# Performance work log

Measured on AMD Instinct MI355X. Metric: run time of the kernel, lower is better.

## Reference

```python
import jax, jax.numpy as jnp
import numpy as np
from jax import lax

EPS = 1e-5


def _bin_act(a):
    # sign binarization of activations (forward value only)
    return jnp.sign(a)


def _bin_weight(w):
    # XNOR-style: per-output-channel scaling alpha = mean(|w|), sign weights
    alpha = jnp.mean(jnp.abs(w), axis=(1, 2, 3), keepdims=True)  # [O,1,1,1]
    return jnp.sign(w) * alpha


def _binconv3x3(a, w, stride=1):
    ba = _bin_act(a)
    bw = _bin_weight(w)
    return lax.conv_general_dilated(
        ba, bw, window_strides=(stride, stride), padding=[(1, 1), (1, 1)],
        dimension_numbers=("NCHW", "OIHW", "NCHW"))


def _bn(x, gamma, beta, mean, var):
    # eval-mode BatchNorm2d with running stats; params shaped [1,C,1,1]
    inv = lax.rsqrt(var + EPS)
    return (x - mean) * inv * gamma + beta


def setup_inputs() -> dict:
    key = jax.random.key(0)
    ks = jax.random.split(key, 18)
    B, C, H, W = 32, 256, 56, 56
    p = lambda k, scale=1.0: jax.random.normal(k, (1, C, 1, 1), jnp.float32) * scale
    return {
        "x": jax.random.normal(ks[0], (B, C, H, W), jnp.float32),
        "sh11": p(ks[1], 0.01), "sh12": p(ks[2], 0.01),
        "w1": jax.random.normal(ks[3], (C, C, 3, 3), jnp.float32) * 0.05,
        "sc1": jax.random.uniform(ks[4], (1, C, 1, 1), jnp.float32) * 0.001,
        "g1": 1.0 + p(ks[5], 0.1), "b1": p(ks[6], 0.1),
        "m1": p(ks[7], 0.1), "v1": 0.5 + jax.random.uniform(ks[8], (1, C, 1, 1), jnp.float32),
        "sh21": p(ks[9], 0.01), "sh22": p(ks[10], 0.01),
        "w2": jax.random.normal(ks[11], (C, C, 3, 3), jnp.float32) * 0.05,
        "sc2": jax.random.uniform(ks[12], (1, C, 1, 1), jnp.float32) * 0.001,
        "g2": 1.0 + p(ks[13], 0.1), "b2": p(ks[14], 0.1),
        "m2": p(ks[15], 0.1), "v2": 0.5 + jax.random.uniform(ks[16], (1, C, 1, 1), jnp.float32),
    }


def reference(x, sh11, sh12, w1, sc1, g1, b1, m1, v1,
              sh21, sh22, w2, sc2, g2, b2, m2, v2):
    # --- sub-block 1 ---
    residual = x
    out1 = _binconv3x3(x + sh11, w1)
    out2 = _binconv3x3(x + sh12, w1)
    out = out1 + sc1 * out2
    out = _bn(out, g1, b1, m1, v1)
    out = out + residual
    out = jnp.clip(out, -1.0, 1.0)  # Hardtanh
    # --- sub-block 2 ---
    residual = out
    out1 = _binconv3x3(out + sh21, w2)
    out2 = _binconv3x3(out + sh22, w2)
    out = out1 + sc2 * out2
    out = _bn(out, g2, b2, m2, v2)
    out = out + residual
    out = jnp.clip(out, -1.0, 1.0)  # Hardtanh
    return out
```

## Files before the change

### kernel.cpp

```cpp
#include <hip/hip_runtime.h>
#include <cstdint>
#include <cstddef>

typedef int v4i __attribute__((ext_vector_type(4)));

#define HWSZ 3136
#define WID 56
#define CCH 256
#define BAT 32
#define NPIX (BAT*HWSZ)
#define KTOT 2304
#define PW 58
#define PIMG (PW*PW)
#define PSZ (BAT*PIMG*64)

static __device__ __forceinline__ uint16_t f2bf(float f) {
    uint32_t x = __float_as_uint(f);
    x += 0x7fffu + ((x >> 16) & 1u);
    return (uint16_t)(x >> 16);
}

static __device__ __forceinline__ void load_lds_16(const void* g, void* l) {
    __builtin_amdgcn_global_load_lds(
        (const __attribute__((address_space(1))) uint32_t*)g,
        (__attribute__((address_space(3))) uint32_t*)l, 16, 0, 0);
}

__global__ void pack_weights(const float* __restrict__ w,
                             const float* __restrict__ sc,
                             const float* __restrict__ g,
                             const float* __restrict__ bb,
                             const float* __restrict__ m,
                             const float* __restrict__ v,
                             int8_t* __restrict__ wpack,
                             float* __restrict__ params) {
    int o = blockIdx.x;
    int t = threadIdx.x;
    const float* wo = w + (size_t)o * KTOT;
    __shared__ float red[256];
    float s = 0.f;
    for (int i = t; i < KTOT; i += 256) {
        float val = wo[i];
        s += fabsf(val);
        int c = i / 9, tap = i - c * 9;
        int8_t sgn = (val > 0.f) ? 1 : ((val < 0.f) ? -1 : 0);
        wpack[(size_t)o * KTOT + tap * 256 + c] = sgn;
    }
    red[t] = s;
    __syncthreads();
    for (int off = 128; off > 0; off >>= 1) {
        if (t < off) red[t] += red[t + off];
        __syncthreads();
    }
    if (t == 0) {
        float alpha = red[0] / (float)KTOT;
        float inv = rsqrtf(v[o] + 1e-5f);
        float cs = alpha * inv * g[o];
        params[o]         = cs;
        params[256 + o]   = cs * sc[o];
        params[512 + o]   = bb[o] - m[o] * inv * g[o];
    }
}

__global__ void halo_zero(int8_t* b0, int8_t* b1, int8_t* b2, int8_t* b3) {
    int bx = blockIdx.x;
    int8_t* bufs[4] = {b0, b1, b2, b3};
    int8_t* buf = bufs[bx >> 5];
    int im = bx & 31;
    v4i z = (v4i){0, 0, 0, 0};
    for (int idx = threadIdx.x; idx < 3648; idx += 256) {
        int plane = idx / 912;
        int rr = idx - plane * 912;
        int pix_i = rr >> 2, c16 = rr & 3;
        int h, w;
        if (pix_i < 58)       { h = 0;  w = pix_i; }
        else if (pix_i < 116) { h = 57; w = pix_i - 58; }
        else if (pix_i < 172) { h = pix_i - 115; w = 0; }
        else                  { h = pix_i - 171; w = 57; }
        size_t off = (size_t)plane * PSZ + (size_t)im * PIMG * 64
                   + (size_t)(h * PW + w) * 64 + c16 * 16;
        *(v4i*)(buf + off) = z;
    }
}

__global__ void binarize_x(const float* __restrict__ x,
                           const float* __restrict__ sh1,
                           const float* __restrict__ sh2,
                           int8_t* __restrict__ a1,
                           int8_t* __restrict__ a2) {
    __shared__ int8_t s1[32][260];
    __shared__ int8_t s2[32][260];
    int b = blockIdx.y;
    int hw0 = blockIdx.x * 32;
    int t = threadIdx.x;
    int hw4 = (t & 7) * 4;
    int crow = t >> 3;
    for (int i = 0; i < 8; ++i) {
        int c = crow + 32 * i;
        float4 val = *(const float4*)(x + ((size_t)(b * CCH + c)) * HWSZ + hw0 + hw4);
        float fA = sh1[c], fB = sh2[c];
        float vv[4] = {val.x, val.y, val.z, val.w};
        for (int j = 0; j < 4; ++j) {
            float u1 = vv[j] + fA;
            float u2 = vv[j] + fB;
            s1[hw4 + j][c] = (u1 > 0.f) ? 1 : ((u1 < 0.f) ? -1 : 0);
            s2[hw4 + j][c] = (u2 > 0.f) ? 1 : ((u2 < 0.f) ? -1 : 0);
        }
    }
    __syncthreads();
    int c4 = (t & 63) * 4;
    int plane = c4 >> 6, cin = c4 & 63;
    for (int j = 0; j < 8; ++j) {
        int hwl = (t >> 6) + 4 * j;
        int hwg = hw0 + hwl;
        int h = hwg / WID, w = hwg - h * WID;
        uchar4 p1 = *(const uchar4*)&s1[hwl][c4];
        uchar4 p2 = *(const uchar4*)&s2[hwl][c4];
        size_t dst = (size_t)plane * PSZ
                   + ((size_t)(b * PIMG) + (size_t)(h + 1) * PW + (w + 1)) * 64 + cin;
        *(uchar4*)(a1 + dst) = p1;
        *(uchar4*)(a2 + dst) = p2;
    }
}

template<int SB>
__global__ __launch_bounds__(256, 5)
void bingemm(const int8_t* __restrict__ a1g,
             const int8_t* __restrict__ a2g,
             const int8_t* __restrict__ wp,
             const float* __restrict__ params,
             const void* __restrict__ res,
             void* __restrict__ outp,
             const float* __restrict__ shA,
             const float* __restrict__ shB,
             int8_t* __restrict__ o1g,
             int8_t* __restrict__ o2g)
{
    __shared__ __align__(16) int8_t sB[2][8192];

    int fid = blockIdx.x;
    int xcd = fid & 7, slot = fid >> 3;
    int o0 = (slot & 3) * 64;
    int m0 = (xcd * 196 + (slot >> 2)) * 64;

    int t = threadIdx.x, lane = t & 63, wv = t >> 6;
    int ml = lane & 15, kc = lane >> 4;

    int apix;
    {
        int pix = m0 + wv * 16 + ml;
        int b = pix / HWSZ, hw = pix - b * HWSZ;
        int h = hw / WID, w = hw - h * WID;
        apix = (b * PIMG + (h + 1) * PW + (w + 1)) * 64 + kc * 16;
    }
    const int8_t* a1p0 = a1g;
    const int8_t* a1p1 = a1g + (size_t)PSZ;
    const int8_t* a1p2 = a1g + 2 * (size_t)PSZ;
    const int8_t* a1p3 = a1g + 3 * (size_t)PSZ;
    const int8_t* a2p0 = a2g;
    const int8_t* a2p1 = a2g + (size_t)PSZ;
    const int8_t* a2p2 = a2g + 2 * (size_t)PSZ;
    const int8_t* a2p3 = a2g + 3 * (size_t)PSZ;

    int brow = t >> 2, bcs = t & 3;
    int bkk = (bcs - (brow >> 1)) & 3;
    const int8_t* bsrc = wp + (size_t)(o0 + brow) * KTOT + (size_t)bkk * 16;
    int rbase = ml * 64 + (((kc + (ml >> 1)) & 3) * 16);

    v4i acc1[4], acc2[4];
    #pragma unroll
    for (int n = 0; n < 4; ++n) {
        acc1[n] = (v4i){0, 0, 0, 0};
        acc2[n] = (v4i){0, 0, 0, 0};
    }

    v4i a1f[2], a2f[2];

    #define ASP(s) ((((s)/12 - 1) * PW + ((s)%3 - 1)) * 64)
    #define A1P(s) ((((s)%12)/3) == 0 ? a1p0 : (((s)%12)/3) == 1 ? a1p1 : (((s)%12)/3) == 2 ? a1p2 : a1p3)
    #define A2P(s) ((((s)%12)/3) == 0 ? a2p0 : (((s)%12)/3) == 1 ? a2p1 : (((s)%12)/3) == 2 ? a2p2 : a2p3)
    #define KOFF(s) ((((s)/12) * 3 + (s)%3) * 256 + (((s)%12)/3) * 64)

    load_lds_16(bsrc + KOFF(0), &sB[0][0 * 4096 + wv * 1024]);
    load_lds_16(bsrc + KOFF(1), &sB[0][1 * 4096 + wv * 1024]);
    __builtin_amdgcn_sched_barrier(0);
    a1f[0] = *(const v4i*)(A1P(0) + apix + ASP(0));
    a2f[0] = *(const v4i*)(A2P(0) + apix + ASP(0));
    a1f[1] = *(const v4i*)(A1P(1) + apix + ASP(1));
    a2f[1] = *(const v4i*)(A2P(1) + apix + ASP(1));
    __builtin_amdgcn_sched_barrier(0);
    asm volatile("s_waitcnt vmcnt(4)");
    __builtin_amdgcn_s_barrier();
    __builtin_amdgcn_sched_barrier(0);

    #pragma unroll
    for (int g = 0; g < 18; ++g) {
        int gb = g & 1;
        if (g < 17) {
            load_lds_16(bsrc + KOFF(2 * g + 2), &sB[gb ^ 1][0 * 4096 + wv * 1024]);
            load_lds_16(bsrc + KOFF(2 * g + 3), &sB[gb ^ 1][1 * 4096 + wv * 1024]);
            __builtin_amdgcn_sched_barrier(0);
        }
        #pragma unroll
        for (int j = 0; j < 2; ++j) {
            int s = 2 * g + j;
            v4i bf[4];
            #pragma unroll
            for (int ns = 0; ns < 4; ++ns)
                bf[ns] = *(const v4i*)&sB[gb][j * 4096 + ns * 1024 + rbase];
            #pragma unroll
            for (int ns = 0; ns < 4; ++ns) {
                acc1[ns] = __builtin_amdgcn_mfma_i32_16x16x64_i8(a1f[j], bf[ns], acc1[ns], 0, 0, 0);
                acc2[ns] = __builtin_amdgcn_mfma_i32_16x16x64_i8(a2f[j], bf[ns], acc2[ns], 0, 0, 0);
            }
            if (g < 17) {
                int sn = s + 2;
                a1f[j] = *(const v4i*)(A1P(sn) + apix + ASP(sn));
                a2f[j] = *(const v4i*)(A2P(sn) + apix + ASP(sn));
            }
            (void)s;
        }
        if (g < 17) {
            __builtin_amdgcn_sched_barrier(0);
            asm volatile("s_waitcnt vmcnt(4)");
            __builtin_amdgcn_s_barrier();
            __builtin_amdgcn_sched_barrier(0);
        }
    }
    #undef ASP
    #undef A1P
    #undef A2P
    #undef KOFF

    int pix0 = m0 + wv * 16 + kc * 4;
    int eb = pix0 / HWSZ, ehw = pix0 - eb * HWSZ;
    #pragma unroll
    for (int ns = 0; ns < 4; ++ns) {
        int o = o0 + ns * 16 + ml;
        float c1 = params[o], c2 = params[256 + o], c3 = params[512 + o];
        float sA = 0.f, sBv = 0.f;
        if (SB == 1) { sA = shA[o]; sBv = shB[o]; }
        size_t rb = ((size_t)(eb * CCH + o)) * HWSZ + ehw;
        float rv[4];
        if (SB == 1) {
            float4 r4 = *(const float4*)((const float*)res + rb);
            rv[0] = r4.x; rv[1] = r4.y; rv[2] = r4.z; rv[3] = r4.w;
        } else {
            ushort4 u = *(const ushort4*)((const uint16_t*)res + rb);
            rv[0] = __uint_as_float((uint32_t)u.x << 16);
            rv[1] = __uint_as_float((uint32_t)u.y << 16);
            rv[2] = __uint_as_float((uint32_t)u.z << 16);
            rv[3] = __uint_as_float((uint32_t)u.w << 16);
        }
        float vals[4];
        #pragma unroll
        for (int r = 0; r < 4; ++r) {
            float v = (float)acc1[ns][r] * c1
                    + (float)acc2[ns][r] * c2 + c3 + rv[r];
            vals[r] = fminf(1.f, fmaxf(-1.f, v));
        }
        if (SB == 1) {
            ushort4 st;
            st.x = f2bf(vals[0]); st.y = f2bf(vals[1]);
            st.z = f2bf(vals[2]); st.w = f2bf(vals[3]);
            *(ushort4*)((uint16_t*)outp + rb) = st;
            int h = ehw / WID, w = ehw - h * WID;
            size_t pp = (size_t)(o0 >> 6) * PSZ
                      + ((size_t)(eb * PIMG) + (size_t)(h + 1) * PW + (w + 1)) * 64
                      + (o & 63);
            #pragma unroll
            for (int r = 0; r < 4; ++r) {
                float u1 = vals[r] + sA, u2 = vals[r] + sBv;
                o1g[pp + (size_t)r * 64] = (u1 > 0.f) ? 1 : ((u1 < 0.f) ? -1 : 0);
                o2g[pp + (size_t)r * 64] = (u2 > 0.f) ? 1 : ((u2 < 0.f) ? -1 : 0);
            }
        } else {
            float4 st = {vals[0], vals[1], vals[2], vals[3]};
            *(float4*)((float*)outp + rb) = st;
        }
    }
}

extern "C" void kernel_launch(void* const* d_in, const int* in_sizes, int n_in,
                              void* d_out, int out_size, void* d_ws, size_t ws_size,
                              hipStream_t stream) {
    const float* x    = (const float*)d_in[0];
    const float* sh11 = (const float*)d_in[1];
    const float* sh12 = (const float*)d_in[2];
    const float* w1   = (const float*)d_in[3];
    const float* sc1  = (const float*)d_in[4];
    const float* g1   = (const float*)d_in[5];
    const float* b1p  = (const float*)d_in[6];
    const float* m1   = (const float*)d_in[7];
    const float* v1   = (const float*)d_in[8];
    const float* sh21 = (const float*)d_in[9];
    const float* sh22 = (const float*)d_in[10];
    const float* w2   = (const float*)d_in[11];
    const float* sc2  = (const float*)d_in[12];
    const float* g2   = (const float*)d_in[13];
    const float* b2p  = (const float*)d_in[14];
    const float* m2   = (const float*)d_in[15];
    const float* v2   = (const float*)d_in[16];

    uint8_t* ws = (uint8_t*)d_ws;
    size_t off = 0;
    auto alloc = [&](size_t bytes) -> uint8_t* {
        uint8_t* p = ws + off;
        off += (bytes + 255) & ~(size_t)255;
        return p;
    };
    const size_t PADB = (size_t)BAT * PIMG * 256;
    int8_t*   a1  = (int8_t*)alloc(PADB);
    int8_t*   a2  = (int8_t*)alloc(PADB);
    int8_t*   bb1 = (int8_t*)alloc(PADB);
    int8_t*   bb2 = (int8_t*)alloc(PADB);
    uint16_t* mid = (uint16_t*)alloc((size_t)NPIX * 256 * 2);
    int8_t*   wp1 = (int8_t*)alloc((size_t)256 * KTOT);
    int8_t*   wp2 = (int8_t*)alloc((size_t)256 * KTOT);
    float*    par1 = (float*)alloc(3 * 256 * 4);
    float*    par2 = (float*)alloc(3 * 256 * 4);
    (void)ws_size; (void)in_sizes; (void)n_in; (void)out_size;

    pack_weights<<<256, 256, 0, stream>>>(w1, sc1, g1, b1p, m1, v1, wp1, par1);
    pack_weights<<<256, 256, 0, stream>>>(w2, sc2, g2, b2p, m2, v2, wp2, par2);
    halo_zero<<<128, 256, 0, stream>>>(a1, a2, bb1, bb2);
    binarize_x<<<dim3(98, 32), 256, 0, stream>>>(x, sh11, sh12, a1, a2);
    bingemm<1><<<6272, 256, 0, stream>>>(a1, a2, wp1, par1, x, mid,
                                         sh21, sh22, bb1, bb2);
    bingemm<2><<<6272, 256, 0, stream>>>(bb1, bb2, wp2, par2, mid, d_out,
                                         nullptr, nullptr, nullptr, nullptr);
}
```

Baseline: 567.0 us.

## Split int8 MFMA main loop into four barrier-separated clusters with priority boosts

Restructures the K loop so each stage is four sub-phases. Each sub-phase loads two B fragments from LDS, issues part of the next global-to-LDS prefetch or A-fragment load, then runs a cluster of four MFMAs under s_setprio(1) between workgroup barriers. The goal is to interleave memory issue with MFMA bursts across waves, a ping-pong style schedule. The cost is many extra s_barrier and lgkmcnt(0) waits per iteration, which may serialize waves and add stalls.

```diff
diff --git a/kernel.cpp b/kernel.cpp
--- a/kernel.cpp
+++ b/kernel.cpp
@@ -123,6 +123,8 @@
     }
 }
 
+#define MFMA_I8(a, b, c) __builtin_amdgcn_mfma_i32_16x16x64_i8((a), (b), (c), 0, 0, 0)
+
 template<int SB>
 __global__ __launch_bounds__(256, 5)
 void bingemm(const int8_t* __restrict__ a1g,
@@ -195,37 +197,84 @@
 
     #pragma unroll
     for (int g = 0; g < 18; ++g) {
-        int gb = g & 1;
+        const int gb = g & 1;
+        int8_t* nb = &sB[gb ^ 1][0];
+        v4i bf0, bf1;
+
+        bf0 = *(const v4i*)&sB[gb][0 * 4096 + 0 * 1024 + rbase];
+        bf1 = *(const v4i*)&sB[gb][0 * 4096 + 1 * 1024 + rbase];
+        if (g < 17) load_lds_16(bsrc + KOFF(2 * g + 2), nb + 0 * 4096 + wv * 1024);
+        __builtin_amdgcn_sched_barrier(0);
+        __builtin_amdgcn_s_barrier();
+        asm volatile("s_waitcnt lgkmcnt(0)");
+        __builtin_amdgcn_sched_barrier(0);
+        __builtin_amdgcn_s_setprio(1);
+        acc1[0] = MFMA_I8(a1f[0], bf0, acc1[0]);
+        acc2[0] = MFMA_I8(a2f[0], bf0, acc2[0]);
+        acc1[1] = MFMA_I8(a1f[0], bf1, acc1[1]);
+        acc2[1] = MFMA_I8(a2f[0], bf1, acc2[1]);
+        __builtin_amdgcn_s_setprio(0);
+        __builtin_amdgcn_sched_barrier(0);
+        __builtin_amdgcn_s_barrier();
+
+        bf0 = *(const v4i*)&sB[gb][0 * 4096 + 2 * 1024 + rbase];
+        bf1 = *(const v4i*)&sB[gb][0 * 4096 + 3 * 1024 + rbase];
+        if (g < 17) load_lds_16(bsrc + KOFF(2 * g + 3), nb + 1 * 4096 + wv * 1024);
+        __builtin_amdgcn_sched_barrier(0);
+        __builtin_amdgcn_s_barrier();
+        asm volatile("s_waitcnt lgkmcnt(0)");
+        __builtin_amdgcn_sched_barrier(0);
+        __builtin_amdgcn_s_setprio(1);
+        acc1[2] = MFMA_I8(a1f[0], bf0, acc1[2]);
+        acc2[2] = MFMA_I8(a2f[0], bf0, acc2[2]);
+        acc1[3] = MFMA_I8(a1f[0], bf1, acc1[3]);
+        acc2[3] = MFMA_I8(a2f[0], bf1, acc2[3]);
+        __builtin_amdgcn_s_setprio(0);
+        __builtin_amdgcn_sched_barrier(0);
+        __builtin_amdgcn_s_barrier();
+
+        bf0 = *(const v4i*)&sB[gb][1 * 4096 + 0 * 1024 + rbase];
+        bf1 = *(const v4i*)&sB[gb][1 * 4096 + 1 * 1024 + rbase];
         if (g < 17) {
-            load_lds_16(bsrc + KOFF(2 * g + 2), &sB[gb ^ 1][0 * 4096 + wv * 1024]);
-            load_lds_16(bsrc + KOFF(2 * g + 3), &sB[gb ^ 1][1 * 4096 + wv * 1024]);
-            __builtin_amdgcn_sched_barrier(0);
-        }
-        #pragma unroll
-        for (int j = 0; j < 2; ++j) {
-            int s = 2 * g + j;
-            v4i bf[4];
-            #pragma unroll
-            for (int ns = 0; ns < 4; ++ns)
-                bf[ns] = *(const v4i*)&sB[gb][j * 4096 + ns * 1024 + rbase];
-            #pragma unroll
-            for (int ns = 0; ns < 4; ++ns) {
-                acc1[ns] = __builtin_amdgcn_mfma_i32_16x16x64_i8(a1f[j], bf[ns], acc1[ns], 0, 0, 0);
-                acc2[ns] = __builtin_amdgcn_mfma_i32_16x16x64_i8(a2f[j], bf[ns], acc2[ns], 0, 0, 0);
-            }
-            if (g < 17) {
-                int sn = s + 2;
-                a1f[j] = *(const v4i*)(A1P(sn) + apix + ASP(sn));
-                a2f[j] = *(const v4i*)(A2P(sn) + apix + ASP(sn));
-            }
-            (void)s;
-        }
+            const int sn = 2 * g + 2;
+            a1f[0] = *(const v4i*)(A1P(sn) + apix + ASP(sn));
+            a2f[0] = *(const v4i*)(A2P(sn) + apix + ASP(sn));
+        }
+        __builtin_amdgcn_sched_barrier(0);
+        __builtin_amdgcn_s_barrier();
+        asm volatile("s_waitcnt lgkmcnt(0)");
+        __builtin_amdgcn_sched_barrier(0);
+        __builtin_amdgcn_s_setprio(1);
+        acc1[0] = MFMA_I8(a1f[1], bf0, acc1[0]);
+        acc2[0] = MFMA_I8(a2f[1], bf0, acc2[0]);
+        acc1[1] = MFMA_I8(a1f[1], bf1, acc1[1]);
+        acc2[1] = MFMA_I8(a2f[1], bf1, acc2[1]);
+        __builtin_amdgcn_s_setprio(0);
+        __builtin_amdgcn_sched_barrier(0);
+        __builtin_amdgcn_s_barrier();
+
+        bf0 = *(const v4i*)&sB[gb][1 * 4096 + 2 * 1024 + rbase];
+        bf1 = *(const v4i*)&sB[gb][1 * 4096 + 3 * 1024 + rbase];
+        __builtin_amdgcn_sched_barrier(0);
+        __builtin_amdgcn_s_barrier();
+        asm volatile("s_waitcnt lgkmcnt(0)");
+        __builtin_amdgcn_sched_barrier(0);
+        __builtin_amdgcn_s_setprio(1);
+        acc1[2] = MFMA_I8(a1f[1], bf0, acc1[2]);
+        acc2[2] = MFMA_I8(a2f[1], bf0, acc2[2]);
+        acc1[3] = MFMA_I8(a1f[1], bf1, acc1[3]);
+        acc2[3] = MFMA_I8(a2f[1], bf1, acc2[3]);
+        __builtin_amdgcn_s_setprio(0);
+        __builtin_amdgcn_sched_barrier(0);
         if (g < 17) {
-            __builtin_amdgcn_sched_barrier(0);
-            asm volatile("s_waitcnt vmcnt(4)");
-            __builtin_amdgcn_s_barrier();
-            __builtin_amdgcn_sched_barrier(0);
-        }
+            const int sn = 2 * g + 3;
+            a1f[1] = *(const v4i*)(A1P(sn) + apix + ASP(sn));
+            a2f[1] = *(const v4i*)(A2P(sn) + apix + ASP(sn));
+        }
+        __builtin_amdgcn_sched_barrier(0);
+        asm volatile("s_waitcnt vmcnt(4)");
+        __builtin_amdgcn_s_barrier();
+        __builtin_amdgcn_sched_barrier(0);
     }
     #undef ASP
     #undef A1P
```

Result: no change. 570.4 us (+0.6%).
